# Kernel tuning notes

Measured on AMD Instinct MI355X. Metric: run time of the kernel, lower is better.

Reference implementation:

```python
import jax, jax.numpy as jnp
import numpy as np

NUM_HEADS = 16


def _bayes_w(mu, rho, eps):
    # reparameterized weight sample: w = mu + softplus(rho) * eps
    return mu + jax.nn.softplus(rho) * eps


def setup_inputs() -> dict:
    key = jax.random.key(0)
    ks = jax.random.split(key, 12)
    B, N, C = 4, 2048, 1024
    x = jax.random.normal(ks[0], (B, N, C), jnp.float32)
    w_scale = 0.02
    q_w = jax.random.normal(ks[1], (C, C), jnp.float32) * w_scale
    k_w = jax.random.normal(ks[2], (C, C), jnp.float32) * w_scale
    v_mu = jax.random.normal(ks[3], (C, C), jnp.float32) * w_scale
    v_rho = jax.random.normal(ks[4], (C, C), jnp.float32) * 0.1 - 3.0
    v_eps = jax.random.normal(ks[5], (C, C), jnp.float32)
    proj_mu = jax.random.normal(ks[6], (C, C), jnp.float32) * w_scale
    proj_rho = jax.random.normal(ks[7], (C, C), jnp.float32) * 0.1 - 3.0
    proj_eps = jax.random.normal(ks[8], (C, C), jnp.float32)
    pb_mu = jax.random.normal(ks[9], (C,), jnp.float32) * w_scale
    pb_rho = jax.random.normal(ks[10], (C,), jnp.float32) * 0.1 - 3.0
    pb_eps = jax.random.normal(ks[11], (C,), jnp.float32)
    return {"x": x, "q_w": q_w, "k_w": k_w, "v_mu": v_mu, "v_rho": v_rho,
            "v_eps": v_eps, "proj_mu": proj_mu, "proj_rho": proj_rho,
            "proj_eps": proj_eps, "pb_mu": pb_mu, "pb_rho": pb_rho,
            "pb_eps": pb_eps}


def reference(x, q_w, k_w, v_mu, v_rho, v_eps, proj_mu, proj_rho, proj_eps,
              pb_mu, pb_rho, pb_eps):
    B, N, C = x.shape
    H = NUM_HEADS
    D = C // H
    scale = D ** -0.5
    v_w = _bayes_w(v_mu, v_rho, v_eps)
    # projections (torch Linear: y = x @ W.T)
    q = (x @ q_w.T).reshape(B, N, H, D).transpose(0, 2, 1, 3)  # [B,H,N,D]
    k = (x @ k_w.T).reshape(B, N, H, D).transpose(0, 2, 1, 3)
    v = (x @ v_w.T).reshape(B, N, H, D).transpose(0, 2, 1, 3)
    attn = jax.nn.softmax(jnp.einsum("bhnd,bhmd->bhnm", q * scale, k), axis=-1)
    out = jnp.einsum("bhnm,bhmd->bhnd", attn, v)
    out = out.transpose(0, 2, 1, 3).reshape(B, N, C)
    p_w = _bayes_w(proj_mu, proj_rho, proj_eps)
    p_b = _bayes_w(pb_mu, pb_rho, pb_eps)
    return out @ p_w.T + p_b
```

## Files before the change

### kernel.cpp

```cpp
#include <hip/hip_runtime.h>
#include <hip/hip_bf16.h>
#include <cstdint>
#include <math.h>

typedef __bf16 bf16;
typedef __bf16 bf16x8 __attribute__((ext_vector_type(8)));
typedef __bf16 bf16x4 __attribute__((ext_vector_type(4)));
typedef float  f32x4 __attribute__((ext_vector_type(4)));

#define LOG2E 1.4426950408889634f

#if __has_builtin(__builtin_amdgcn_exp2f)
#define EXP2(x) __builtin_amdgcn_exp2f(x)
#else
#define EXP2(x) exp2f(x)
#endif

#define AS1 __attribute__((address_space(1)))
#define AS3 __attribute__((address_space(3)))

__device__ __forceinline__ void gload_lds16(const bf16* g, bf16* l) {
    __builtin_amdgcn_global_load_lds((AS1 void*)g, (AS3 void*)l, 16, 0, 0);
}

__device__ __forceinline__ float softplus_f(float r) {
    return (r > 15.f) ? r : log1pf(expf(r));
}

__global__ __launch_bounds__(256)
void prep_kernel(const float* __restrict__ x, bf16* __restrict__ xb,
                 const float* __restrict__ q_w, const float* __restrict__ k_w,
                 bf16* __restrict__ wqkv,
                 const float* __restrict__ v_mu, const float* __restrict__ v_rho,
                 const float* __restrict__ v_eps,
                 const float* __restrict__ p_mu, const float* __restrict__ p_rho,
                 const float* __restrict__ p_eps, bf16* __restrict__ pwb,
                 const float* __restrict__ pb_mu, const float* __restrict__ pb_rho,
                 const float* __restrict__ pb_eps, float* __restrict__ p_b) {
    const int Wsz = 1024 * 1024;
    int blk = blockIdx.x;
    if (blk < 8192) {
        int i = blk * 256 + threadIdx.x;
        float4 v = ((const float4*)x)[i];
        bf16 o[4] = {(bf16)v.x, (bf16)v.y, (bf16)v.z, (bf16)v.w};
        *(uint64_t*)&xb[i * 4] = *(uint64_t*)o;
    } else if (blk < 10240) {
        const float* src = (blk < 9216) ? q_w : k_w;
        bf16* dst = (blk < 9216) ? wqkv : wqkv + Wsz;
        int i = ((blk - 8192) & 1023) * 256 + threadIdx.x;
        float4 v = ((const float4*)src)[i];
        bf16 o[4] = {(bf16)v.x, (bf16)v.y, (bf16)v.z, (bf16)v.w};
        *(uint64_t*)&dst[i * 4] = *(uint64_t*)o;
    } else if (blk < 12288) {
        const bool isv = blk < 11264;
        const float* mu  = isv ? v_mu  : p_mu;
        const float* rho = isv ? v_rho : p_rho;
        const float* eps = isv ? v_eps : p_eps;
        bf16* dst = isv ? wqkv + 2 * Wsz : pwb;
        int i = ((blk - 10240) & 1023) * 256 + threadIdx.x;
        float4 m = ((const float4*)mu)[i];
        float4 r = ((const float4*)rho)[i];
        float4 e = ((const float4*)eps)[i];
        bf16 o[4] = {(bf16)(m.x + softplus_f(r.x) * e.x),
                     (bf16)(m.y + softplus_f(r.y) * e.y),
                     (bf16)(m.z + softplus_f(r.z) * e.z),
                     (bf16)(m.w + softplus_f(r.w) * e.w)};
        *(uint64_t*)&dst[i * 4] = *(uint64_t*)o;
    } else {
        int i = threadIdx.x;
        float4 m = ((const float4*)pb_mu)[i];
        float4 r = ((const float4*)pb_rho)[i];
        float4 e = ((const float4*)pb_eps)[i];
        float4 o;
        o.x = m.x + softplus_f(r.x) * e.x;
        o.y = m.y + softplus_f(r.y) * e.y;
        o.z = m.z + softplus_f(r.z) * e.z;
        o.w = m.w + softplus_f(r.w) * e.w;
        ((float4*)p_b)[i] = o;
    }
}

template <typename OutT>
__global__ __launch_bounds__(256)
void gemm_bt(const bf16* __restrict__ A, const bf16* __restrict__ W,
             OutT* __restrict__ C, const float* __restrict__ bias,
             int M, int N, int K, float q_scale, int q_cols) {
    __shared__ bf16 lA[128 * 32];
    __shared__ bf16 lB[128 * 32];

    const int lane = threadIdx.x & 63;
    const int wv   = threadIdx.x >> 6;
    const int wr   = wv >> 1, wc = wv & 1;

    const int nwg = gridDim.x * gridDim.y;
    int bidl = blockIdx.y * gridDim.x + blockIdx.x;
    if ((nwg & 7) == 0) bidl = (bidl & 7) * (nwg >> 3) + (bidl >> 3);
    const int m0 = (bidl / gridDim.x) * 128, n0 = (bidl % gridDim.x) * 128;

    const int col = lane & 15, quad = lane >> 4;
    const float scale = (n0 < q_cols) ? q_scale : 1.0f;

    const int srow  = wv * 16 + (lane >> 2);
    const int skcol = (lane & 3) * 8;

    f32x4 acc[4][4] = {};

    for (int k0 = 0; k0 < K; k0 += 32) {
#pragma unroll
        for (int r = 0; r < 2; ++r) {
            gload_lds16(A + (size_t)(m0 + r * 64 + srow) * K + k0 + skcol,
                        &lA[(r * 64 + wv * 16) * 32]);
            gload_lds16(W + (size_t)(n0 + r * 64 + srow) * K + k0 + skcol,
                        &lB[(r * 64 + wv * 16) * 32]);
        }
        __syncthreads();

        bf16x8 af[4], bfr[4];
#pragma unroll
        for (int t = 0; t < 4; ++t) {
            af[t]  = *(const bf16x8*)&lA[(wr * 64 + t * 16 + col) * 32 + quad * 8];
            bfr[t] = *(const bf16x8*)&lB[(wc * 64 + t * 16 + col) * 32 + quad * 8];
        }
#pragma unroll
        for (int i = 0; i < 4; ++i)
#pragma unroll
            for (int j = 0; j < 4; ++j)
                acc[i][j] = __builtin_amdgcn_mfma_f32_16x16x32_bf16(af[i], bfr[j], acc[i][j], 0, 0, 0);
        __syncthreads();
    }

#pragma unroll
    for (int i = 0; i < 4; ++i) {
        int row = m0 + wr * 64 + i * 16 + quad * 4;
#pragma unroll
        for (int j = 0; j < 4; ++j) {
            int cc = n0 + wc * 64 + j * 16 + col;
            float bv = bias ? bias[cc] : 0.f;
#pragma unroll
            for (int r = 0; r < 4; ++r)
                C[(size_t)(row + r) * N + cc] = (OutT)(acc[i][j][r] * scale + bv);
        }
    }
}

#define SWZ(row, ec) ((row) * 64 + ((ec) ^ (((row) & 7) << 3)))

__global__ __launch_bounds__(256, 2)
void attn_kernel(const bf16* __restrict__ QKV, bf16* __restrict__ O) {
    __shared__ bf16 sK[2][64 * 64];
    __shared__ bf16 sVt[64 * 64];
    __shared__ bf16 sP [256 * 64];

    const int lane = threadIdx.x & 63;
    const int wv   = threadIdx.x >> 6;
    const int col  = lane & 15, quad = lane >> 4;

    const int bid  = blockIdx.x;
    const int work = (bid & 7) * 64 + (bid >> 3);
    const int qt = work & 7, h = (work >> 3) & 15, b = work >> 7;

    const size_t rowQ0 = (size_t)b * 2048 + qt * 256;
    const bf16* Qg = QKV + rowQ0 * 3072 + h * 64;
    const bf16* Kg = QKV + (size_t)b * 2048 * 3072 + 1024 + h * 64;
    const bf16* Vg = QKV + (size_t)b * 2048 * 3072 + 2048 + h * 64;

    const int rloc = lane >> 3;
    const bf16* Kdma = Kg + (size_t)(wv * 16 + rloc) * 3072 + (((lane & 7) ^ rloc) * 8);

    gload_lds16(Kdma,                    &sK[0][(wv * 16) * 64]);
    gload_lds16(Kdma + (size_t)8 * 3072, &sK[0][(wv * 16 + 8) * 64]);

    const int dc0 = wv * 8, dc1 = 32 + wv * 8;
    bf16x8 vr0 = *(const bf16x8*)&Vg[(size_t)lane * 3072 + dc0];
    bf16x8 vr1 = *(const bf16x8*)&Vg[(size_t)lane * 3072 + dc1];

#pragma unroll
    for (int it = 0; it < 8; ++it) {
        int c = it * 256 + threadIdx.x;
        int row = c >> 3, ec = (c & 7) * 8;
        *(bf16x8*)&sP[SWZ(row, ec)] = *(const bf16x8*)&Qg[(size_t)row * 3072 + ec];
    }
    __syncthreads();
    bf16x8 qf[4][2];
#pragma unroll
    for (int mi = 0; mi < 4; ++mi)
#pragma unroll
        for (int ks = 0; ks < 2; ++ks)
            qf[mi][ks] = *(const bf16x8*)&sP[SWZ(wv * 64 + mi * 16 + col, ks * 32 + quad * 8)];

    f32x4 lsum[4] = {};
    f32x4 o[4][4] = {};
    const int cx = col & 7;

    for (int t = 0; t < 32; ++t) {
        const int p = t & 1;

#pragma unroll
        for (int j = 0; j < 8; ++j) sVt[SWZ(dc0 + j, lane)] = vr0[j];
#pragma unroll
        for (int j = 0; j < 8; ++j) sVt[SWZ(dc1 + j, lane)] = vr1[j];
        __syncthreads();

        if (t < 31) {
            const bf16* kn = Kdma + (size_t)(t * 64 + 64) * 3072;
            gload_lds16(kn,                    &sK[p ^ 1][(wv * 16) * 64]);
            gload_lds16(kn + (size_t)8 * 3072, &sK[p ^ 1][(wv * 16 + 8) * 64]);
        }

        bf16x8 kf0[4], kf1[4];
#pragma unroll
        for (int nj = 0; nj < 4; ++nj) {
            kf0[nj] = *(const bf16x8*)&sK[p][(nj * 16 + col) * 64 + ((quad ^ cx) * 8)];
            kf1[nj] = *(const bf16x8*)&sK[p][(nj * 16 + col) * 64 + (((quad ^ cx) ^ 4) * 8)];
        }

#pragma unroll
        for (int mi = 0; mi < 4; ++mi) {
            f32x4 st[4];
            __builtin_amdgcn_s_setprio(1);
#pragma unroll
            for (int nj = 0; nj < 4; ++nj) {
                f32x4 tacc = {0.f, 0.f, 0.f, 0.f};
                tacc = __builtin_amdgcn_mfma_f32_16x16x32_bf16(kf0[nj], qf[mi][0], tacc, 0, 0, 0);
                tacc = __builtin_amdgcn_mfma_f32_16x16x32_bf16(kf1[nj], qf[mi][1], tacc, 0, 0, 0);
                st[nj] = tacc;
            }
            __builtin_amdgcn_s_setprio(0);
#pragma unroll
            for (int nj = 0; nj < 4; ++nj) {
                f32x4 pv;
#pragma unroll
                for (int r = 0; r < 4; ++r) pv[r] = EXP2(st[nj][r]);
                lsum[mi] += pv;
                bf16x4 pk = {(bf16)pv[0], (bf16)pv[1], (bf16)pv[2], (bf16)pv[3]};
                *(bf16x4*)&sP[SWZ(wv * 64 + mi * 16 + col, nj * 16 + quad * 4)] = pk;
            }
        }

        if (t < 31) {
            const bf16* vn = Vg + (size_t)(t * 64 + 64 + lane) * 3072;
            vr0 = *(const bf16x8*)&vn[dc0];
            vr1 = *(const bf16x8*)&vn[dc1];
        }

        __builtin_amdgcn_s_setprio(1);
#pragma unroll
        for (int ks = 0; ks < 2; ++ks) {
            bf16x8 pf[4];
#pragma unroll
            for (int mi = 0; mi < 4; ++mi)
                pf[mi] = *(const bf16x8*)&sP[SWZ(wv * 64 + mi * 16 + col, ks * 32 + quad * 8)];
#pragma unroll
            for (int dj = 0; dj < 4; ++dj) {
                bf16x8 vf = *(const bf16x8*)&sVt[SWZ(dj * 16 + col, ks * 32 + quad * 8)];
#pragma unroll
                for (int mi = 0; mi < 4; ++mi)
                    o[mi][dj] = __builtin_amdgcn_mfma_f32_16x16x32_bf16(pf[mi], vf, o[mi][dj], 0, 0, 0);
            }
        }
        __builtin_amdgcn_s_setprio(0);
        __syncthreads();
    }

#pragma unroll
    for (int mi = 0; mi < 4; ++mi) {
        float l = lsum[mi][0] + lsum[mi][1] + lsum[mi][2] + lsum[mi][3];
        l += __shfl_xor(l, 16, 64);
        l += __shfl_xor(l, 32, 64);
#pragma unroll
        for (int r = 0; r < 4; ++r) {
            float inv = 1.f / __shfl(l, quad * 4 + r, 64);
            size_t row = rowQ0 + wv * 64 + mi * 16 + quad * 4 + r;
#pragma unroll
            for (int dj = 0; dj < 4; ++dj)
                O[row * 1024 + h * 64 + dj * 16 + col] = (bf16)(o[mi][dj][r] * inv);
        }
    }
}

extern "C" void kernel_launch(void* const* d_in, const int* in_sizes, int n_in,
                              void* d_out, int out_size, void* d_ws, size_t ws_size,
                              hipStream_t stream) {
    const float* x      = (const float*)d_in[0];
    const float* q_w    = (const float*)d_in[1];
    const float* k_w    = (const float*)d_in[2];
    const float* v_mu   = (const float*)d_in[3];
    const float* v_rho  = (const float*)d_in[4];
    const float* v_eps  = (const float*)d_in[5];
    const float* p_mu   = (const float*)d_in[6];
    const float* p_rho  = (const float*)d_in[7];
    const float* p_eps  = (const float*)d_in[8];
    const float* pb_mu  = (const float*)d_in[9];
    const float* pb_rho = (const float*)d_in[10];
    const float* pb_eps = (const float*)d_in[11];
    float* out = (float*)d_out;

    const size_t MB = (size_t)1 << 20;
    char* ws = (char*)d_ws;
    bf16*  xb   = (bf16*)(ws);
    bf16*  wqkv = (bf16*)(ws + 16 * MB);
    bf16*  pwb  = (bf16*)(ws + 22 * MB);
    float* p_b  = (float*)(ws + 24 * MB);
    bf16*  QKV  = (bf16*)(ws + 25 * MB);
    bf16*  Ab   = xb;

    prep_kernel<<<12289, 256, 0, stream>>>(x, xb, q_w, k_w, wqkv,
                                           v_mu, v_rho, v_eps,
                                           p_mu, p_rho, p_eps, pwb,
                                           pb_mu, pb_rho, pb_eps, p_b);

    gemm_bt<bf16><<<dim3(24, 64), 256, 0, stream>>>(xb, wqkv, QKV, nullptr,
                                                    8192, 3072, 1024, 0.125f * LOG2E, 1024);

    attn_kernel<<<dim3(512), 256, 0, stream>>>(QKV, Ab);

    gemm_bt<float><<<dim3(8, 64), 256, 0, stream>>>(Ab, pwb, out, p_b,
                                                    8192, 1024, 1024, 1.0f, 1024);
}
```

Before: 301.4 us.

## Rewrite GEMM with 128x256 tiles, double-buffered LDS and swizzled layout

Replaces the single-buffered 128x128 GEMM (K step 32) with an 8-wave 512-thread kernel that computes 128x256 tiles with a K step of 64. It double-buffers the LDS tiles so the next tile's global-to-LDS loads overlap the current MFMAs. It also XOR-swizzles the LDS layout to reduce bank conflicts and raises wave priority around the MFMA bursts. The grids shrink to 12x64 and 4x64 blocks, which reduces occupancy and wave count, particularly for the output projection (256 blocks).

```diff
diff --git a/kernel.cpp b/kernel.cpp
--- a/kernel.cpp
+++ b/kernel.cpp
@@ -81,64 +81,90 @@
 }
 
 template <typename OutT>
-__global__ __launch_bounds__(256)
-void gemm_bt(const bf16* __restrict__ A, const bf16* __restrict__ W,
-             OutT* __restrict__ C, const float* __restrict__ bias,
-             int M, int N, int K, float q_scale, int q_cols) {
-    __shared__ bf16 lA[128 * 32];
-    __shared__ bf16 lB[128 * 32];
-
-    const int lane = threadIdx.x & 63;
-    const int wv   = threadIdx.x >> 6;
-    const int wr   = wv >> 1, wc = wv & 1;
+__global__ __launch_bounds__(512, 2)
+void gemm_bt8(const bf16* __restrict__ A, const bf16* __restrict__ W,
+              OutT* __restrict__ C, const float* __restrict__ bias,
+              int M, int N, int K, float q_scale, int q_cols) {
+    __shared__ bf16 sA[2][128 * 64];
+    __shared__ bf16 sB[2][256 * 64];
+
+    const int lane  = threadIdx.x & 63;
+    const int wv    = threadIdx.x >> 6;
+    const int wr    = wv >> 2;
+    const int wc    = wv & 3;
+    const int col16 = lane & 15, quad = lane >> 4;
 
     const int nwg = gridDim.x * gridDim.y;
     int bidl = blockIdx.y * gridDim.x + blockIdx.x;
     if ((nwg & 7) == 0) bidl = (bidl & 7) * (nwg >> 3) + (bidl >> 3);
-    const int m0 = (bidl / gridDim.x) * 128, n0 = (bidl % gridDim.x) * 128;
-
-    const int col = lane & 15, quad = lane >> 4;
+    const int m0 = (bidl / gridDim.x) * 128;
+    const int n0 = (bidl % gridDim.x) * 256;
+
+    const int st_r = lane >> 2;
+    const int st_c = ((lane & 3) * 8) ^ (((lane >> 5) & 1) << 4);
+    const bf16* Asrc = A + (size_t)(m0 + wv * 16 + st_r) * K + st_c;
+    const bf16* Bsrc = W + (size_t)(n0 + wv * 32 + st_r) * K + st_c;
+    const size_t B16K = (size_t)16 * K;
+
+    const int lp = col16 * 32 + ((quad * 8) ^ (((col16 >> 3) & 1) << 4));
+
+    f32x4 acc[4][4] = {};
+    const int NT = K >> 6;
+
+    {
+        gload_lds16(Asrc,             &sA[0][(wv * 2 + 0) * 512]);
+        gload_lds16(Asrc + 32,        &sA[0][(wv * 2 + 1) * 512]);
+        gload_lds16(Bsrc,             &sB[0][(wv * 4 + 0) * 512]);
+        gload_lds16(Bsrc + 32,        &sB[0][(wv * 4 + 1) * 512]);
+        gload_lds16(Bsrc + B16K,      &sB[0][(wv * 4 + 2) * 512]);
+        gload_lds16(Bsrc + B16K + 32, &sB[0][(wv * 4 + 3) * 512]);
+    }
+    __syncthreads();
+
+    for (int t = 0; t < NT; ++t) {
+        const int d = t & 1;
+        if (t + 1 < NT) {
+            const int k0 = (t + 1) << 6;
+            gload_lds16(Asrc + k0,             &sA[d ^ 1][(wv * 2 + 0) * 512]);
+            gload_lds16(Asrc + k0 + 32,        &sA[d ^ 1][(wv * 2 + 1) * 512]);
+            gload_lds16(Bsrc + k0,             &sB[d ^ 1][(wv * 4 + 0) * 512]);
+            gload_lds16(Bsrc + k0 + 32,        &sB[d ^ 1][(wv * 4 + 1) * 512]);
+            gload_lds16(Bsrc + B16K + k0,      &sB[d ^ 1][(wv * 4 + 2) * 512]);
+            gload_lds16(Bsrc + B16K + k0 + 32, &sB[d ^ 1][(wv * 4 + 3) * 512]);
+        }
+#pragma unroll
+        for (int ks = 0; ks < 2; ++ks) {
+            bf16x8 afr[4], bfr[4];
+#pragma unroll
+            for (int m = 0; m < 4; ++m)
+                afr[m] = *(const bf16x8*)&sA[d][((wr * 4 + m) * 2 + ks) * 512 + lp];
+#pragma unroll
+            for (int n = 0; n < 4; ++n)
+                bfr[n] = *(const bf16x8*)&sB[d][((wc * 4 + n) * 2 + ks) * 512 + lp];
+            __builtin_amdgcn_s_barrier();
+            __builtin_amdgcn_s_setprio(1);
+#pragma unroll
+            for (int m = 0; m < 4; ++m)
+#pragma unroll
+                for (int n = 0; n < 4; ++n)
+                    acc[m][n] = __builtin_amdgcn_mfma_f32_16x16x32_bf16(afr[m], bfr[n], acc[m][n], 0, 0, 0);
+            __builtin_amdgcn_s_setprio(0);
+            if (ks == 0) __builtin_amdgcn_s_barrier();
+        }
+        __syncthreads();
+    }
+
     const float scale = (n0 < q_cols) ? q_scale : 1.0f;
-
-    const int srow  = wv * 16 + (lane >> 2);
-    const int skcol = (lane & 3) * 8;
-
-    f32x4 acc[4][4] = {};
-
-    for (int k0 = 0; k0 < K; k0 += 32) {
-#pragma unroll
-        for (int r = 0; r < 2; ++r) {
-            gload_lds16(A + (size_t)(m0 + r * 64 + srow) * K + k0 + skcol,
-                        &lA[(r * 64 + wv * 16) * 32]);
-            gload_lds16(W + (size_t)(n0 + r * 64 + srow) * K + k0 + skcol,
-                        &lB[(r * 64 + wv * 16) * 32]);
-        }
-        __syncthreads();
-
-        bf16x8 af[4], bfr[4];
-#pragma unroll
-        for (int t = 0; t < 4; ++t) {
-            af[t]  = *(const bf16x8*)&lA[(wr * 64 + t * 16 + col) * 32 + quad * 8];
-            bfr[t] = *(const bf16x8*)&lB[(wc * 64 + t * 16 + col) * 32 + quad * 8];
-        }
-#pragma unroll
-        for (int i = 0; i < 4; ++i)
-#pragma unroll
-            for (int j = 0; j < 4; ++j)
-                acc[i][j] = __builtin_amdgcn_mfma_f32_16x16x32_bf16(af[i], bfr[j], acc[i][j], 0, 0, 0);
-        __syncthreads();
-    }
-
-#pragma unroll
-    for (int i = 0; i < 4; ++i) {
-        int row = m0 + wr * 64 + i * 16 + quad * 4;
-#pragma unroll
-        for (int j = 0; j < 4; ++j) {
-            int cc = n0 + wc * 64 + j * 16 + col;
+#pragma unroll
+    for (int m = 0; m < 4; ++m) {
+        int row = m0 + wr * 64 + m * 16 + quad * 4;
+#pragma unroll
+        for (int n = 0; n < 4; ++n) {
+            int cc = n0 + wc * 64 + n * 16 + col16;
             float bv = bias ? bias[cc] : 0.f;
 #pragma unroll
             for (int r = 0; r < 4; ++r)
-                C[(size_t)(row + r) * N + cc] = (OutT)(acc[i][j][r] * scale + bv);
+                C[(size_t)(row + r) * N + cc] = (OutT)(acc[m][n][r] * scale + bv);
         }
     }
 }
@@ -309,11 +335,11 @@
                                            p_mu, p_rho, p_eps, pwb,
                                            pb_mu, pb_rho, pb_eps, p_b);
 
-    gemm_bt<bf16><<<dim3(24, 64), 256, 0, stream>>>(xb, wqkv, QKV, nullptr,
-                                                    8192, 3072, 1024, 0.125f * LOG2E, 1024);
+    gemm_bt8<bf16><<<dim3(12, 64), 512, 0, stream>>>(xb, wqkv, QKV, nullptr,
+                                                     8192, 3072, 1024, 0.125f * LOG2E, 1024);
 
     attn_kernel<<<dim3(512), 256, 0, stream>>>(QKV, Ab);
 
-    gemm_bt<float><<<dim3(8, 64), 256, 0, stream>>>(Ab, pwb, out, p_b,
-                                                    8192, 1024, 1024, 1.0f, 1024);
-}
+    gemm_bt8<float><<<dim3(4, 64), 512, 0, stream>>>(Ab, pwb, out, p_b,
+                                                     8192, 1024, 1024, 1.0f, 1024);
+}
```

After: 316.2 us. 1.05x slower.
